# Performance work log

Measured on AMD Instinct MI355X. Metric: run time of the kernel, lower is better.

## Reference

```python
import jax, jax.numpy as jnp
import numpy as np

B, SEQ_LEN, CHANNELS, PRED_LEN = 64, 1024, 512, 720
KERNEL = 25
PAD = (KERNEL - 1) // 2  # 12
IN_LEN = SEQ_LEN // 2    # 512
INV_SQRT2 = 1.0 / np.sqrt(2.0).astype(np.float32)


def dct2_ortho_matrix(N):
    # Orthonormal DCT-II basis: X_k = s_k * sum_n x_n cos(pi*(n+0.5)*k/N)
    n = np.arange(N, dtype=np.float64)
    k = np.arange(N, dtype=np.float64)
    M = np.cos(np.pi * (n[None, :] + 0.5) * k[:, None] / N)
    scale = np.sqrt(2.0 / N) * np.ones(N)
    scale[0] = np.sqrt(1.0 / N)
    return jnp.asarray((scale[:, None] * M).astype(np.float32))  # [k, n]


def setup_inputs() -> dict:
    key = jax.random.key(0)
    k1, k2, k3, k4, k5 = jax.random.split(key, 5)
    bound = 1.0 / np.sqrt(IN_LEN)
    return {
        "x": jax.random.normal(k1, (B, SEQ_LEN, CHANNELS), dtype=jnp.float32),
        "W_seasonal": jax.random.uniform(k2, (PRED_LEN, IN_LEN), jnp.float32, -bound, bound),
        "b_seasonal": jax.random.uniform(k3, (PRED_LEN,), jnp.float32, -bound, bound),
        "W_trend": jax.random.uniform(k4, (PRED_LEN, IN_LEN), jnp.float32, -bound, bound),
        "b_trend": jax.random.uniform(k5, (PRED_LEN,), jnp.float32, -bound, bound),
    }


def reference(x, W_seasonal, b_seasonal, W_trend, b_trend):
    # --- series decomposition: moving average (edge-padded, window 25) ---
    padded = jnp.pad(x, ((0, 0), (PAD, PAD), (0, 0)), mode="edge")  # [B, L+24, C]
    cs = jnp.cumsum(padded, axis=1)
    cs = jnp.pad(cs, ((0, 0), (1, 0), (0, 0)))  # leading zero, [B, L+25, C]
    trend = (cs[:, KERNEL:, :] - cs[:, :-KERNEL, :]) / KERNEL  # [B, L, C]
    seasonal = x - trend

    # [B, C, L]
    s = jnp.transpose(seasonal, (0, 2, 1))
    t = jnp.transpose(trend, (0, 2, 1))

    # --- grouped conv1d with [1,1]/sqrt(2), stride 2 (Haar low-pass downsample) ---
    def down(v):
        return (v[..., 0::2] + v[..., 1::2]) * INV_SQRT2  # [B, C, L/2]

    s = down(s)
    t = down(t)

    # --- orthonormal DCT-II over last axis, then divide by length ---
    Mdct = dct2_ortho_matrix(IN_LEN)  # [k, n]
    s = jnp.einsum("bcn,kn->bck", s, Mdct) / IN_LEN
    t = jnp.einsum("bcn,kn->bck", t, Mdct) / IN_LEN

    # --- shared Linear per branch ---
    s_out = jnp.einsum("bck,pk->bcp", s, W_seasonal) + b_seasonal
    t_out = jnp.einsum("bck,pk->bcp", t, W_trend) + b_trend

    out = s_out + t_out  # [B, C, pred_len]
    return jnp.transpose(out, (0, 2, 1))  # [B, pred_len, C]
```

## Files before the change

### kernel.cpp

```cpp
#include <hip/hip_runtime.h>
#include <hip/hip_bf16.h>
#include <math.h>


#define BATCH 64
#define SEQ 1024
#define CH 512
#define PRED 720
#define INV_SQRT2 0.70710678118654752440f

typedef __attribute__((ext_vector_type(4))) float floatx4;
typedef __attribute__((ext_vector_type(8))) short bf16x8;

#define KBF_OFF   0ull
#define BIAS_OFF  1572864ull
#define MW_OFF    1575936ull
#define WEFFS_OFF 2624512ull
#define WEFFT_OFF 4099072ull
#define XT_OFF    5573632ull
#define WS_NEED   (XT_OFF + 67108864ull)

__global__ void __launch_bounds__(256) build_weff(
    const float* __restrict__ Ws_in, const float* __restrict__ Wt_in,
    float* __restrict__ outS, float* __restrict__ outT) {
    const float* W = blockIdx.z ? Wt_in : Ws_in;
    float* out     = blockIdx.z ? outT  : outS;
    int n0 = blockIdx.x * 64;
    int p0 = blockIdx.y * 64;
    int t  = threadIdx.x;
    int tx = t & 15, ty = t >> 4;
    __shared__ float wlds[32][65];
    __shared__ float mlds[32][64];
    float a[4][4] = {};
    for (int kb = 0; kb < 512; kb += 32) {
        __syncthreads();
        {
            int pp = t >> 2, kk0 = (t & 3) * 8;
            int prow = min(p0 + pp, PRED - 1);
            const float* wsrc = &W[(size_t)prow * 512 + kb + kk0];
#pragma unroll
            for (int e = 0; e < 8; e++) wlds[kk0 + e][pp] = wsrc[e];
        }
        {
            int kk = t >> 3, nn0 = (t & 7) * 8;
            int k = kb + kk;
            float scale = (k == 0) ? 0.04419417382415922f
                                   : 0.0625f;
            scale *= (1.0f / 512.0f);
#pragma unroll
            for (int e = 0; e < 8; e++) {
                int n = n0 + nn0 + e;
                int m = ((2 * n + 1) * k) & 2047;
                float ang = (float)m * (float)(M_PI / 1024.0);
                mlds[kk][nn0 + e] = cosf(ang) * scale;
            }
        }
        __syncthreads();
#pragma unroll
        for (int kk = 0; kk < 32; kk++) {
            floatx4 wv = *reinterpret_cast<const floatx4*>(&wlds[kk][ty * 4]);
            floatx4 mv = *reinterpret_cast<const floatx4*>(&mlds[kk][tx * 4]);
#pragma unroll
            for (int i = 0; i < 4; i++)
#pragma unroll
                for (int j = 0; j < 4; j++)
                    a[i][j] += wv[i] * mv[j];
        }
    }
#pragma unroll
    for (int i = 0; i < 4; i++) {
        int p = p0 + ty * 4 + i;
        if (p < PRED) {
            floatx4 v = {a[i][0], a[i][1], a[i][2], a[i][3]};
            *reinterpret_cast<floatx4*>(&out[(size_t)p * 512 + n0 + tx * 4]) = v;
        }
    }
}

__device__ __forceinline__ int tcnt(int j, int l) {
    if (l == 0)    return max(0, 13 - j);
    if (l == 1023) return max(0, j - 1010);
    int d = l - j; if (d < 0) d = -d;
    return (d <= 12) ? 1 : 0;
}

__global__ void build_kmat(const float* __restrict__ Ws, const float* __restrict__ Wt,
                           const float* __restrict__ bs, const float* __restrict__ bt,
                           __hip_bfloat16* __restrict__ Kbf, float* __restrict__ bias) {
    int idx = blockIdx.x * 256 + threadIdx.x;
    int p = idx >> 10, l = idx & 1023;
    if (p >= PRED) { Kbf[idx] = __float2bfloat16(0.0f); return; }
    if (l == 0) bias[p] = bs[p] + bt[p];
    float v = INV_SQRT2 * Ws[(size_t)p * 512 + (l >> 1)];
    int jlo = max(0, l - 12), jhi = min(1023, l + 12);
    float acc = 0.f;
    for (int n = (jlo >> 1); n <= (jhi >> 1); n++) {
        int c = tcnt(2 * n, l) + tcnt(2 * n + 1, l);
        if (c) acc += (Wt[(size_t)p * 512 + n] - Ws[(size_t)p * 512 + n]) * (float)c;
    }
    v += acc * (INV_SQRT2 / 25.0f);
    Kbf[idx] = __float2bfloat16(v);
}

__device__ __forceinline__ void async_ld16(const void* g, void* l) {
    __builtin_amdgcn_global_load_lds((const __attribute__((address_space(1))) void*)g,
                                     (__attribute__((address_space(3))) void*)l, 16, 0, 0);
}

__device__ __forceinline__ short f2bf(float f) {
    __hip_bfloat16 h = __float2bfloat16(f);
    return *reinterpret_cast<short*>(&h);
}

__global__ void __launch_bounds__(256) xpose(const float* __restrict__ x,
                                             short* __restrict__ xT) {
    __shared__ float lds[64][65];
    int t = threadIdx.x;
    int l0 = blockIdx.x * 64, c0 = blockIdx.y * 64, b = blockIdx.z;
    const float* xb = x + (size_t)b * SEQ * CH;
    int row4 = t >> 4, cq = t & 15;
#pragma unroll
    for (int i = 0; i < 4; i++) {
        int row = row4 + i * 16;
        floatx4 v = __builtin_nontemporal_load(reinterpret_cast<const floatx4*>(
            xb + (size_t)(l0 + row) * CH + c0 + cq * 4));
#pragma unroll
        for (int e = 0; e < 4; e++) lds[row][cq * 4 + e] = v[e];
    }
    __syncthreads();
    size_t outb = (size_t)b * CH * SEQ;
#pragma unroll
    for (int r = 0; r < 2; r++) {
        int u = r * 256 + t;
        int lr = u & 7, c = u >> 3;
        bf16x8 s;
#pragma unroll
        for (int e = 0; e < 8; e++) s[e] = f2bf(lds[lr * 8 + e][c]);
        *reinterpret_cast<bf16x8*>(&xT[outb + (size_t)(c0 + c) * SEQ + l0 + lr * 8]) = s;
    }
}

__global__ void __launch_bounds__(512, 2) gemm_main_t(
    const short* __restrict__ Kbf, const short* __restrict__ xT,
    const float* __restrict__ bias, float* __restrict__ out) {
    __shared__ __align__(16) short ldsbuf[3 * 24576];
    int t = threadIdx.x;
    int wave = t >> 6, lane = t & 63;
    int bid = blockIdx.x;
    int work = (bid & 7) * 96 + (bid >> 3);
    int mt = work % 6;
    int nt = work / 6;
    int wm = wave >> 2, wn = wave & 3;
    const short* Ag = Kbf + (size_t)mt * 128 * 1024;
    const short* Bg = xT + (size_t)nt * 256 * 1024;

    size_t so[4];
#pragma unroll
    for (int a = 0; a < 4; a++) {
        int s = a * 512 + t;
        so[a] = (size_t)(((s >> 7) << 4) + (s & 15)) * 1024
              + ((s >> 6) & 1) * 32 + ((s >> 4) & 3) * 8;
    }

    floatx4 acc[4][4];
#pragma unroll
    for (int i = 0; i < 4; i++)
#pragma unroll
        for (int j = 0; j < 4; j++)
            acc[i][j] = (floatx4){0.f, 0.f, 0.f, 0.f};

#define STAGE(bufidx, k0v)                                                     \
    {                                                                          \
        char* base_ = (char*)ldsbuf + (bufidx) * 49152;                        \
        _Pragma("unroll")                                                      \
        for (int a = 0; a < 2; a++)                                            \
            async_ld16(Ag + so[a] + (k0v),                                     \
                       base_ + (a * 512 + wave * 64) * 16);                    \
        _Pragma("unroll")                                                      \
        for (int a = 0; a < 4; a++)                                            \
            async_ld16(Bg + so[a] + (k0v),                                     \
                       base_ + 16384 + (a * 512 + wave * 64) * 16);            \
    }

    STAGE(0, 0);
    STAGE(1, 64);

    int cur = 0, nx2 = 2;
    for (int it = 0; it < 15; ++it) {
        asm volatile("s_waitcnt vmcnt(6)" ::: "memory");
        __builtin_amdgcn_s_barrier();
        __builtin_amdgcn_sched_barrier(0);
        if (it < 14) STAGE(nx2, (it + 2) * 64);
        const char* cb = (const char*)ldsbuf + cur * 49152;
#pragma unroll
        for (int ks = 0; ks < 2; ks++) {
            bf16x8 af[4], bf[4];
#pragma unroll
            for (int i = 0; i < 4; i++)
                af[i] = *reinterpret_cast<const bf16x8*>(
                    cb + ((wm * 4 + i) << 11) + (ks << 10) + (lane << 4));
#pragma unroll
            for (int j = 0; j < 4; j++)
                bf[j] = *reinterpret_cast<const bf16x8*>(
                    cb + 16384 + ((wn * 4 + j) << 11) + (ks << 10) + (lane << 4));
            __builtin_amdgcn_s_setprio(1);
#pragma unroll
            for (int i = 0; i < 4; i++)
#pragma unroll
                for (int j = 0; j < 4; j++)
                    acc[i][j] = __builtin_amdgcn_mfma_f32_16x16x32_bf16(af[i], bf[j], acc[i][j], 0, 0, 0);
            __builtin_amdgcn_s_setprio(0);
        }
        cur = (cur == 2) ? 0 : cur + 1;
        nx2 = (nx2 == 2) ? 0 : nx2 + 1;
    }
    asm volatile("s_waitcnt vmcnt(0)" ::: "memory");
    __builtin_amdgcn_s_barrier();
    __builtin_amdgcn_sched_barrier(0);
    {
        const char* cb = (const char*)ldsbuf + cur * 49152;
#pragma unroll
        for (int ks = 0; ks < 2; ks++) {
            bf16x8 af[4], bf[4];
#pragma unroll
            for (int i = 0; i < 4; i++)
                af[i] = *reinterpret_cast<const bf16x8*>(
                    cb + ((wm * 4 + i) << 11) + (ks << 10) + (lane << 4));
#pragma unroll
            for (int j = 0; j < 4; j++)
                bf[j] = *reinterpret_cast<const bf16x8*>(
                    cb + 16384 + ((wn * 4 + j) << 11) + (ks << 10) + (lane << 4));
#pragma unroll
            for (int i = 0; i < 4; i++)
#pragma unroll
                for (int j = 0; j < 4; j++)
                    acc[i][j] = __builtin_amdgcn_mfma_f32_16x16x32_bf16(af[i], bf[j], acc[i][j], 0, 0, 0);
        }
    }
#undef STAGE

    int lm = lane & 15, kq = lane >> 4;
    int p0r = mt * 128 + wm * 64;
    int b   = nt >> 1;
    int cb2 = (nt & 1) * 256 + wn * 64 + lm;
    size_t outb = (size_t)b * PRED * CH;
#pragma unroll
    for (int i = 0; i < 4; i++) {
#pragma unroll
        for (int r = 0; r < 4; r++) {
            int p = p0r + i * 16 + kq * 4 + r;
            if (p < PRED) {
                float bv = bias[p];
#pragma unroll
                for (int j = 0; j < 4; j++)
                    __builtin_nontemporal_store(acc[i][j][r] + bv,
                                                &out[outb + (size_t)p * CH + cb2 + j * 16]);
            }
        }
    }
}

__global__ void __launch_bounds__(256) gemm_main(
    const short* __restrict__ Kbf, const float* __restrict__ x,
    const float* __restrict__ bias, float* __restrict__ out) {
    __shared__ __align__(16) short ldsA[128 * 32];
    int t = threadIdx.x;
    int wave = t >> 6, lane = t & 63;
    int mt = blockIdx.x % 6, nt = blockIdx.x / 6;
    int b  = blockIdx.y;
    int wm = wave >> 1, wn = wave & 1;
    const short* Ag = Kbf + (size_t)mt * 128 * 1024;
    const float* xb = x + (size_t)b * SEQ * CH;
    int lm = lane & 15, kq = lane >> 4;
    int cj[4];
    for (int j = 0; j < 4; j++) cj[j] = nt * 128 + wn * 64 + j * 16 + lm;

    floatx4 acc[4][4];
    for (int i = 0; i < 4; i++)
        for (int j = 0; j < 4; j++)
            acc[i][j] = (floatx4){0.f, 0.f, 0.f, 0.f};

    for (int k0 = 0; k0 < 1024; k0 += 32) {
        for (int rdi = 0; rdi < 2; rdi++) {
            int q = rdi * 256 + t;
            int row = q >> 2, ko = (q & 3) * 8;
            async_ld16(Ag + (size_t)row * 1024 + k0 + ko,
                       (char*)ldsA + rdi * 4096 + wave * 1024);
        }
        bf16x8 bfrag[4];
        int krow = k0 + kq * 8;
#pragma unroll
        for (int j = 0; j < 4; j++) {
            const float* xc = xb + (size_t)krow * CH + cj[j];
            bf16x8 bv;
#pragma unroll
            for (int i = 0; i < 8; i++) bv[i] = f2bf(xc[(size_t)i * CH]);
            bfrag[j] = bv;
        }
        __syncthreads();
        bf16x8 af[4];
        for (int i = 0; i < 4; i++)
            af[i] = *(const bf16x8*)&ldsA[(wm * 64 + i * 16 + lm) * 32 + kq * 8];
        for (int i = 0; i < 4; i++)
            for (int j = 0; j < 4; j++)
                acc[i][j] = __builtin_amdgcn_mfma_f32_16x16x32_bf16(af[i], bfrag[j], acc[i][j], 0, 0, 0);
        __syncthreads();
    }

    int p0 = mt * 128 + wm * 64;
    size_t outb = (size_t)b * PRED * CH;
    for (int i = 0; i < 4; i++) {
        for (int r = 0; r < 4; r++) {
            int p = p0 + i * 16 + kq * 4 + r;
            if (p < PRED) {
                float bv = bias[p];
                for (int j = 0; j < 4; j++) {
                    out[outb + (size_t)p * CH + cj[j]] = acc[i][j][r] + bv;
                }
            }
        }
    }
}

extern "C" void kernel_launch(void* const* d_in, const int* in_sizes, int n_in,
                              void* d_out, int out_size, void* d_ws, size_t ws_size,
                              hipStream_t stream) {
    const float* xp = nullptr; const float* wp[2] = {nullptr, nullptr};
    const float* bp[2] = {nullptr, nullptr};
    int wn = 0, bn = 0;
    for (int i = 0; i < n_in; i++) {
        if (in_sizes[i] == 33554432) xp = (const float*)d_in[i];
        else if (in_sizes[i] == 368640 && wn < 2) wp[wn++] = (const float*)d_in[i];
        else if (in_sizes[i] == 720 && bn < 2) bp[bn++] = (const float*)d_in[i];
    }
    if (!xp || wn != 2 || bn != 2) {
        xp = (const float*)d_in[0]; wp[0] = (const float*)d_in[1];
        bp[0] = (const float*)d_in[2]; wp[1] = (const float*)d_in[3];
        bp[1] = (const float*)d_in[4];
    }
    float* out = (float*)d_out;

    char* ws = (char*)d_ws;
    __hip_bfloat16* Kbf = (__hip_bfloat16*)(ws + KBF_OFF);
    float* bias  = (float*)(ws + BIAS_OFF);
    float* WeffS = (float*)(ws + WEFFS_OFF);
    float* WeffT = (float*)(ws + WEFFT_OFF);
    short* xT    = (short*)(ws + XT_OFF);

    bool big = (ws_size >= (size_t)WS_NEED);

    if (big) xpose<<<dim3(16, 8, 64), 256, 0, stream>>>(xp, xT);
    build_weff<<<dim3(8, 12, 2), 256, 0, stream>>>(wp[0], wp[1], WeffS, WeffT);
    build_kmat<<<3072, 256, 0, stream>>>(WeffS, WeffT, bp[0], bp[1], Kbf, bias);
    if (big)
        gemm_main_t<<<768, 512, 0, stream>>>((const short*)Kbf, (const short*)xT, bias, out);
    else
        gemm_main<<<dim3(24, 64), 256, 0, stream>>>((const short*)Kbf, xp, bias, out);
}
```

Before: 349.7 us.

## Enlarge GEMM tile to 256x256 with double buffering and fuse prep kernels

```diff
diff --git a/kernel.cpp b/kernel.cpp
--- a/kernel.cpp
+++ b/kernel.cpp
@@ -14,65 +14,105 @@
 
 #define KBF_OFF   0ull
 #define BIAS_OFF  1572864ull
-#define MW_OFF    1575936ull
 #define WEFFS_OFF 2624512ull
 #define WEFFT_OFF 4099072ull
 #define XT_OFF    5573632ull
 #define WS_NEED   (XT_OFF + 67108864ull)
 
-__global__ void __launch_bounds__(256) build_weff(
+__device__ __forceinline__ void async_ld16(const void* g, void* l) {
+    __builtin_amdgcn_global_load_lds((const __attribute__((address_space(1))) void*)g,
+                                     (__attribute__((address_space(3))) void*)l, 16, 0, 0);
+}
+
+__device__ __forceinline__ short f2bf(float f) {
+    __hip_bfloat16 h = __float2bfloat16(f);
+    return *reinterpret_cast<short*>(&h);
+}
+
+__global__ void __launch_bounds__(256) prep1(
+    const float* __restrict__ x, short* __restrict__ xT,
     const float* __restrict__ Ws_in, const float* __restrict__ Wt_in,
     float* __restrict__ outS, float* __restrict__ outT) {
-    const float* W = blockIdx.z ? Wt_in : Ws_in;
-    float* out     = blockIdx.z ? outT  : outS;
-    int n0 = blockIdx.x * 64;
-    int p0 = blockIdx.y * 64;
-    int t  = threadIdx.x;
-    int tx = t & 15, ty = t >> 4;
-    __shared__ float wlds[32][65];
-    __shared__ float mlds[32][64];
-    float a[4][4] = {};
-    for (int kb = 0; kb < 512; kb += 32) {
+    __shared__ __align__(16) char smem[64 * 65 * 4];
+    int t = threadIdx.x;
+    int nx = (int)gridDim.x - 192;
+    if ((int)blockIdx.x < nx) {
+        float (*lds)[65] = reinterpret_cast<float(*)[65]>(smem);
+        int idx = blockIdx.x;
+        int l0 = (idx & 15) * 64, c0 = ((idx >> 4) & 7) * 64, b = idx >> 7;
+        const float* xb = x + (size_t)b * SEQ * CH;
+        int row4 = t >> 4, cq = t & 15;
+#pragma unroll
+        for (int i = 0; i < 4; i++) {
+            int row = row4 + i * 16;
+            floatx4 v = __builtin_nontemporal_load(reinterpret_cast<const floatx4*>(
+                xb + (size_t)(l0 + row) * CH + c0 + cq * 4));
+#pragma unroll
+            for (int e = 0; e < 4; e++) lds[row][cq * 4 + e] = v[e];
+        }
         __syncthreads();
-        {
-            int pp = t >> 2, kk0 = (t & 3) * 8;
-            int prow = min(p0 + pp, PRED - 1);
-            const float* wsrc = &W[(size_t)prow * 512 + kb + kk0];
-#pragma unroll
-            for (int e = 0; e < 8; e++) wlds[kk0 + e][pp] = wsrc[e];
-        }
-        {
-            int kk = t >> 3, nn0 = (t & 7) * 8;
-            int k = kb + kk;
-            float scale = (k == 0) ? 0.04419417382415922f
-                                   : 0.0625f;
-            scale *= (1.0f / 512.0f);
-#pragma unroll
-            for (int e = 0; e < 8; e++) {
-                int n = n0 + nn0 + e;
-                int m = ((2 * n + 1) * k) & 2047;
-                float ang = (float)m * (float)(M_PI / 1024.0);
-                mlds[kk][nn0 + e] = cosf(ang) * scale;
-            }
-        }
-        __syncthreads();
-#pragma unroll
-        for (int kk = 0; kk < 32; kk++) {
-            floatx4 wv = *reinterpret_cast<const floatx4*>(&wlds[kk][ty * 4]);
-            floatx4 mv = *reinterpret_cast<const floatx4*>(&mlds[kk][tx * 4]);
-#pragma unroll
-            for (int i = 0; i < 4; i++)
-#pragma unroll
-                for (int j = 0; j < 4; j++)
-                    a[i][j] += wv[i] * mv[j];
-        }
-    }
-#pragma unroll
-    for (int i = 0; i < 4; i++) {
-        int p = p0 + ty * 4 + i;
-        if (p < PRED) {
-            floatx4 v = {a[i][0], a[i][1], a[i][2], a[i][3]};
-            *reinterpret_cast<floatx4*>(&out[(size_t)p * 512 + n0 + tx * 4]) = v;
+        size_t outb = (size_t)b * CH * SEQ;
+#pragma unroll
+        for (int r = 0; r < 2; r++) {
+            int u = r * 256 + t;
+            int lr = u & 7, c = u >> 3;
+            bf16x8 s;
+#pragma unroll
+            for (int e = 0; e < 8; e++) s[e] = f2bf(lds[lr * 8 + e][c]);
+            *reinterpret_cast<bf16x8*>(&xT[outb + (size_t)(c0 + c) * SEQ + l0 + lr * 8]) = s;
+        }
+    } else {
+        float (*wlds)[65] = reinterpret_cast<float(*)[65]>(smem);
+        float (*mlds)[64] = reinterpret_cast<float(*)[64]>(smem + 32 * 65 * 4);
+        int wb = (int)blockIdx.x - nx;
+        const float* W = (wb >= 96) ? Wt_in : Ws_in;
+        float* out     = (wb >= 96) ? outT  : outS;
+        int wz = wb % 96;
+        int n0 = (wz & 7) * 64;
+        int p0 = (wz >> 3) * 64;
+        int tx = t & 15, ty = t >> 4;
+        float a[4][4] = {};
+        for (int kb = 0; kb < 512; kb += 32) {
+            __syncthreads();
+            {
+                int pp = t >> 2, kk0 = (t & 3) * 8;
+                int prow = min(p0 + pp, PRED - 1);
+                const float* wsrc = &W[(size_t)prow * 512 + kb + kk0];
+#pragma unroll
+                for (int e = 0; e < 8; e++) wlds[kk0 + e][pp] = wsrc[e];
+            }
+            {
+                int kk = t >> 3, nn0 = (t & 7) * 8;
+                int k = kb + kk;
+                float scale = (k == 0) ? 0.04419417382415922f : 0.0625f;
+                scale *= (1.0f / 512.0f);
+#pragma unroll
+                for (int e = 0; e < 8; e++) {
+                    int n = n0 + nn0 + e;
+                    int m = ((2 * n + 1) * k) & 2047;
+                    float ang = (float)m * (float)(M_PI / 1024.0);
+                    mlds[kk][nn0 + e] = cosf(ang) * scale;
+                }
+            }
+            __syncthreads();
+#pragma unroll
+            for (int kk = 0; kk < 32; kk++) {
+                floatx4 wv = *reinterpret_cast<const floatx4*>(&wlds[kk][ty * 4]);
+                floatx4 mv = *reinterpret_cast<const floatx4*>(&mlds[kk][tx * 4]);
+#pragma unroll
+                for (int i = 0; i < 4; i++)
+#pragma unroll
+                    for (int j = 0; j < 4; j++)
+                        a[i][j] += wv[i] * mv[j];
+            }
+        }
+#pragma unroll
+        for (int i = 0; i < 4; i++) {
+            int p = p0 + ty * 4 + i;
+            if (p < PRED) {
+                floatx4 v = {a[i][0], a[i][1], a[i][2], a[i][3]};
+                *reinterpret_cast<floatx4*>(&out[(size_t)p * 512 + n0 + tx * 4]) = v;
+            }
         }
     }
 }
@@ -102,56 +142,18 @@
     Kbf[idx] = __float2bfloat16(v);
 }
 
-__device__ __forceinline__ void async_ld16(const void* g, void* l) {
-    __builtin_amdgcn_global_load_lds((const __attribute__((address_space(1))) void*)g,
-                                     (__attribute__((address_space(3))) void*)l, 16, 0, 0);
-}
-
-__device__ __forceinline__ short f2bf(float f) {
-    __hip_bfloat16 h = __float2bfloat16(f);
-    return *reinterpret_cast<short*>(&h);
-}
-
-__global__ void __launch_bounds__(256) xpose(const float* __restrict__ x,
-                                             short* __restrict__ xT) {
-    __shared__ float lds[64][65];
-    int t = threadIdx.x;
-    int l0 = blockIdx.x * 64, c0 = blockIdx.y * 64, b = blockIdx.z;
-    const float* xb = x + (size_t)b * SEQ * CH;
-    int row4 = t >> 4, cq = t & 15;
-#pragma unroll
-    for (int i = 0; i < 4; i++) {
-        int row = row4 + i * 16;
-        floatx4 v = __builtin_nontemporal_load(reinterpret_cast<const floatx4*>(
-            xb + (size_t)(l0 + row) * CH + c0 + cq * 4));
-#pragma unroll
-        for (int e = 0; e < 4; e++) lds[row][cq * 4 + e] = v[e];
-    }
-    __syncthreads();
-    size_t outb = (size_t)b * CH * SEQ;
-#pragma unroll
-    for (int r = 0; r < 2; r++) {
-        int u = r * 256 + t;
-        int lr = u & 7, c = u >> 3;
-        bf16x8 s;
-#pragma unroll
-        for (int e = 0; e < 8; e++) s[e] = f2bf(lds[lr * 8 + e][c]);
-        *reinterpret_cast<bf16x8*>(&xT[outb + (size_t)(c0 + c) * SEQ + l0 + lr * 8]) = s;
-    }
-}
-
 __global__ void __launch_bounds__(512, 2) gemm_main_t(
     const short* __restrict__ Kbf, const short* __restrict__ xT,
     const float* __restrict__ bias, float* __restrict__ out) {
-    __shared__ __align__(16) short ldsbuf[3 * 24576];
+    __shared__ __align__(16) short ldsbuf[2 * 32768];
     int t = threadIdx.x;
     int wave = t >> 6, lane = t & 63;
     int bid = blockIdx.x;
-    int work = (bid & 7) * 96 + (bid >> 3);
-    int mt = work % 6;
-    int nt = work / 6;
+    int work = (bid & 7) * 48 + (bid >> 3);
+    int mt = work % 3;
+    int nt = work / 3;
     int wm = wave >> 2, wn = wave & 3;
-    const short* Ag = Kbf + (size_t)mt * 128 * 1024;
+    const short* Ag = Kbf + (size_t)mt * 256 * 1024;
     const short* Bg = xT + (size_t)nt * 256 * 1024;
 
     size_t so[4];
@@ -162,90 +164,81 @@
               + ((s >> 6) & 1) * 32 + ((s >> 4) & 3) * 8;
     }
 
-    floatx4 acc[4][4];
-#pragma unroll
-    for (int i = 0; i < 4; i++)
+    floatx4 acc[8][4];
+#pragma unroll
+    for (int i = 0; i < 8; i++)
 #pragma unroll
         for (int j = 0; j < 4; j++)
             acc[i][j] = (floatx4){0.f, 0.f, 0.f, 0.f};
 
 #define STAGE(bufidx, k0v)                                                     \
     {                                                                          \
-        char* base_ = (char*)ldsbuf + (bufidx) * 49152;                        \
+        char* base_ = (char*)ldsbuf + (bufidx) * 65536;                        \
         _Pragma("unroll")                                                      \
-        for (int a = 0; a < 2; a++)                                            \
-            async_ld16(Ag + so[a] + (k0v),                                     \
-                       base_ + (a * 512 + wave * 64) * 16);                    \
+        for (int a = 0; a < 4; a++)                                            \
+            async_ld16(Ag + so[a] + (k0v), base_ + a * 8192 + wave * 1024);    \
         _Pragma("unroll")                                                      \
         for (int a = 0; a < 4; a++)                                            \
             async_ld16(Bg + so[a] + (k0v),                                     \
-                       base_ + 16384 + (a * 512 + wave * 64) * 16);            \
+                       base_ + 32768 + a * 8192 + wave * 1024);                \
+    }
+
+#define COMPUTE(cbp)                                                           \
+    {                                                                          \
+        _Pragma("unroll")                                                      \
+        for (int ks = 0; ks < 2; ks++) {                                       \
+            bf16x8 af[8], bf[4];                                               \
+            _Pragma("unroll")                                                  \
+            for (int i = 0; i < 8; i++)                                        \
+                af[i] = *reinterpret_cast<const bf16x8*>(                      \
+                    (cbp) + ((wm * 8 + i) << 11) + (ks << 10) + (lane << 4));  \
+            _Pragma("unroll")                                                  \
+            for (int j = 0; j < 4; j++)                                        \
+                bf[j] = *reinterpret_cast<const bf16x8*>(                      \
+                    (cbp) + 32768 + ((wn * 4 + j) << 11) + (ks << 10) +        \
+                    (lane << 4));                                              \
+            __builtin_amdgcn_s_setprio(1);                                     \
+            _Pragma("unroll")                                                  \
+            for (int i = 0; i < 8; i++)                                        \
+                _Pragma("unroll")                                              \
+                for (int j = 0; j < 4; j++)                                    \
+                    acc[i][j] = __builtin_amdgcn_mfma_f32_16x16x32_bf16(       \
+                        af[i], bf[j], acc[i][j], 0, 0, 0);                     \
+            __builtin_amdgcn_s_setprio(0);                                     \
+        }                                                                      \
     }
 
     STAGE(0, 0);
     STAGE(1, 64);
 
-    int cur = 0, nx2 = 2;
     for (int it = 0; it < 15; ++it) {
-        asm volatile("s_waitcnt vmcnt(6)" ::: "memory");
+        asm volatile("s_waitcnt vmcnt(8)" ::: "memory");
         __builtin_amdgcn_s_barrier();
         __builtin_amdgcn_sched_barrier(0);
-        if (it < 14) STAGE(nx2, (it + 2) * 64);
-        const char* cb = (const char*)ldsbuf + cur * 49152;
-#pragma unroll
-        for (int ks = 0; ks < 2; ks++) {
-            bf16x8 af[4], bf[4];
-#pragma unroll
-            for (int i = 0; i < 4; i++)
-                af[i] = *reinterpret_cast<const bf16x8*>(
-                    cb + ((wm * 4 + i) << 11) + (ks << 10) + (lane << 4));
-#pragma unroll
-            for (int j = 0; j < 4; j++)
-                bf[j] = *reinterpret_cast<const bf16x8*>(
-                    cb + 16384 + ((wn * 4 + j) << 11) + (ks << 10) + (lane << 4));
-            __builtin_amdgcn_s_setprio(1);
-#pragma unroll
-            for (int i = 0; i < 4; i++)
-#pragma unroll
-                for (int j = 0; j < 4; j++)
-                    acc[i][j] = __builtin_amdgcn_mfma_f32_16x16x32_bf16(af[i], bf[j], acc[i][j], 0, 0, 0);
-            __builtin_amdgcn_s_setprio(0);
-        }
-        cur = (cur == 2) ? 0 : cur + 1;
-        nx2 = (nx2 == 2) ? 0 : nx2 + 1;
+        const char* cbp = (const char*)ldsbuf + (it & 1) * 65536;
+        COMPUTE(cbp);
+        __builtin_amdgcn_sched_barrier(0);
+        __builtin_amdgcn_s_barrier();
+        __builtin_amdgcn_sched_barrier(0);
+        if (it < 14) STAGE(it & 1, (it + 2) * 64);
     }
     asm volatile("s_waitcnt vmcnt(0)" ::: "memory");
     __builtin_amdgcn_s_barrier();
     __builtin_amdgcn_sched_barrier(0);
     {
-        const char* cb = (const char*)ldsbuf + cur * 49152;
-#pragma unroll
-        for (int ks = 0; ks < 2; ks++) {
-            bf16x8 af[4], bf[4];
-#pragma unroll
-            for (int i = 0; i < 4; i++)
-                af[i] = *reinterpret_cast<const bf16x8*>(
-                    cb + ((wm * 4 + i) << 11) + (ks << 10) + (lane << 4));
-#pragma unroll
-            for (int j = 0; j < 4; j++)
-                bf[j] = *reinterpret_cast<const bf16x8*>(
-                    cb + 16384 + ((wn * 4 + j) << 11) + (ks << 10) + (lane << 4));
-#pragma unroll
-            for (int i = 0; i < 4; i++)
-#pragma unroll
-                for (int j = 0; j < 4; j++)
-                    acc[i][j] = __builtin_amdgcn_mfma_f32_16x16x32_bf16(af[i], bf[j], acc[i][j], 0, 0, 0);
-        }
+        const char* cbp = (const char*)ldsbuf + 65536;
+        COMPUTE(cbp);
     }
 #undef STAGE
+#undef COMPUTE
 
     int lm = lane & 15, kq = lane >> 4;
-    int p0r = mt * 128 + wm * 64;
+    int p0r = mt * 256 + wm * 128;
     int b   = nt >> 1;
     int cb2 = (nt & 1) * 256 + wn * 64 + lm;
     size_t outb = (size_t)b * PRED * CH;
 #pragma unroll
-    for (int i = 0; i < 4; i++) {
+    for (int i = 0; i < 8; i++) {
 #pragma unroll
         for (int r = 0; r < 4; r++) {
             int p = p0r + i * 16 + kq * 4 + r;
@@ -349,11 +342,10 @@
 
     bool big = (ws_size >= (size_t)WS_NEED);
 
-    if (big) xpose<<<dim3(16, 8, 64), 256, 0, stream>>>(xp, xT);
-    build_weff<<<dim3(8, 12, 2), 256, 0, stream>>>(wp[0], wp[1], WeffS, WeffT);
+    prep1<<<(big ? 8192 + 192 : 192), 256, 0, stream>>>(xp, xT, wp[0], wp[1], WeffS, WeffT);
     build_kmat<<<3072, 256, 0, stream>>>(WeffS, WeffT, bp[0], bp[1], Kbf, bias);
     if (big)
-        gemm_main_t<<<768, 512, 0, stream>>>((const short*)Kbf, (const short*)xT, bias, out);
+        gemm_main_t<<<384, 512, 0, stream>>>((const short*)Kbf, (const short*)xT, bias, out);
     else
         gemm_main<<<dim3(24, 64), 256, 0, stream>>>((const short*)Kbf, xp, bias, out);
 }
```

Measured after the change: 421.0 us. 20.4% more time.
